# Optimization experiments

Measured on AMD Instinct MI355X. Metric: run time of the kernel, lower is better.

## Reference

```python
import jax, jax.numpy as jnp
import numpy as np

IN_CH = 256
OUT_CH = 256
K = 3
STRIDE = 1
PAD = 1
NUM_EMB = 8


def setup_inputs() -> dict:
    key = jax.random.key(0)
    ks = jax.random.split(key, 6)
    B, H, W = 16, 64, 64
    x = jax.random.normal(ks[0], (B, IN_CH, H, W), dtype=jnp.float32)
    kernal_embed = jax.random.normal(ks[1], (NUM_EMB, IN_CH, OUT_CH, K, K), dtype=jnp.float32)
    # 1x1 conv params (stored as a dense [out,in] matrix) + bias
    cls_conv_w = jax.random.normal(ks[2], (IN_CH, IN_CH), dtype=jnp.float32) / np.sqrt(IN_CH)
    cls_conv_b = jax.random.normal(ks[3], (IN_CH,), dtype=jnp.float32) * 0.01
    cls_dense_w = jax.random.normal(ks[4], (NUM_EMB, IN_CH), dtype=jnp.float32) / np.sqrt(IN_CH)
    cls_dense_b = jax.random.normal(ks[5], (NUM_EMB,), dtype=jnp.float32) * 0.01
    return {"x": x, "kernal_embed": kernal_embed, "cls_conv_w": cls_conv_w,
            "cls_conv_b": cls_conv_b, "cls_dense_w": cls_dense_w, "cls_dense_b": cls_dense_b}


def reference(x, kernal_embed, cls_conv_w, cls_conv_b, cls_dense_w, cls_dense_b):
    B, C, H, W = x.shape
    # 1x1 conv -> global avg pool -> dense -> softmax weights over embeddings
    w = jnp.einsum('bchw,dc->bdhw', x, cls_conv_w) + cls_conv_b[None, :, None, None]
    pooled = jnp.mean(w, axis=(2, 3))                       # (B, C)
    logits = pooled @ cls_dense_w.T + cls_dense_b           # (B, E)
    mix = jax.nn.softmax(logits, axis=1)                    # (B, E)
    # Per-sample kernel synthesis: (B, in, out, k, k)
    kern = jnp.einsum('be,eiojk->biojk', mix, kernal_embed)
    # Faithful to torch .view(-1, in, k, k): raw reshape (mixes in/out axes as in original)
    kern = kern.reshape(B, OUT_CH, IN_CH, K, K)
    # Grouped conv with groups=B == per-sample conv via vmap
    def conv1(xi, wi):
        # xi: (C, H, W), wi: (out, in, k, k)
        return jax.lax.conv_general_dilated(
            xi[None], wi, window_strides=(STRIDE, STRIDE),
            padding=[(PAD, PAD), (PAD, PAD)],
            dimension_numbers=('NCHW', 'OIHW', 'NCHW'))[0]
    out = jax.vmap(conv1)(x, kern)                          # (B, out, H, W)
    return out
```

## Files before the change

kernel.cpp:

```cpp
#include <hip/hip_runtime.h>
#include <stdint.h>

#define B_  16
#define C_  256
#define H_  64
#define W_  64
#define P_  4096
#define E_  8
#define HP_ 66

typedef __bf16 bf16x8 __attribute__((ext_vector_type(8)));
typedef float  f32x4  __attribute__((ext_vector_type(4)));

__device__ __forceinline__ unsigned short f2bf(float f) {
    union { float f; unsigned int u; } v; v.f = f;
    unsigned int u = v.u;
    unsigned int r = (u + 0x7fffu + ((u >> 16) & 1u)) >> 16;
    return (unsigned short)r;
}

__device__ __forceinline__ void async_load16(const void* g, void* l) {
    __builtin_amdgcn_global_load_lds(
        (const __attribute__((address_space(1))) void*)g,
        (__attribute__((address_space(3))) void*)l, 16, 0, 0);
}

__global__ void k_xpose(const float* __restrict__ x, unsigned short* __restrict__ Xp,
                        float* __restrict__ xsum) {
    const int bid = blockIdx.x;
    const int tid = threadIdx.x;

    if (bid < 520) {
        const int gid = bid * 256 + tid;
        const int pix = gid >> 5;
        const int chunk = gid & 31;
        const int bb = pix / 260;
        const int j = pix - bb * 260;
        int h, w;
        if (j < 66)       { h = 0;  w = j; }
        else if (j < 132) { h = 65; w = j - 66; }
        else { int jj = j - 132; h = 1 + (jj & 63); w = (jj < 64) ? 0 : 65; }
        const uint4 z = {0u, 0u, 0u, 0u};
        *(uint4*)(Xp + ((size_t)((bb * HP_ + h) * HP_ + w) << 8) + chunk * 8) = z;
    }

    const int b  = bid >> 8;
    const int h  = (bid >> 2) & 63;
    const int cg = bid & 3;
    const int c0 = cg << 6;
    __shared__ float tile[64][65];
    {
        const int ci = tid >> 2, wseg = tid & 3;
        const float* src = x + ((size_t)(b * 256 + c0 + ci) << 12) + (h << 6) + wseg * 16;
        float s = 0.f;
#pragma unroll
        for (int i = 0; i < 4; ++i) {
            float4 v = *(const float4*)(src + i * 4);
            tile[ci][wseg * 16 + i * 4 + 0] = v.x;
            tile[ci][wseg * 16 + i * 4 + 1] = v.y;
            tile[ci][wseg * 16 + i * 4 + 2] = v.z;
            tile[ci][wseg * 16 + i * 4 + 3] = v.w;
            s += v.x + v.y + v.z + v.w;
        }
        s += __shfl_down(s, 1, 64);
        s += __shfl_down(s, 2, 64);
        if ((tid & 3) == 0) atomicAdd(&xsum[b * 256 + c0 + ci], s);
    }
    __syncthreads();
    {
        const int w = tid >> 2, cs = tid & 3;
        unsigned short ov[16] __attribute__((aligned(16)));
#pragma unroll
        for (int k = 0; k < 16; ++k) ov[k] = f2bf(tile[cs * 16 + k][w]);
        unsigned short* dst = Xp + ((size_t)((b * HP_ + h + 1) * HP_ + (w + 1)) << 8) + c0 + cs * 16;
        ((uint4*)dst)[0] = ((const uint4*)ov)[0];
        ((uint4*)dst)[1] = ((const uint4*)ov)[1];
    }
}

__global__ void k_mix(const float* __restrict__ xsum,
                      const float* __restrict__ cw, const float* __restrict__ cb,
                      const float* __restrict__ dw, const float* __restrict__ db,
                      float* __restrict__ mix) {
    const int b = blockIdx.x, tid = threadIdx.x;
    __shared__ __align__(16) float sxm[256];
    __shared__ __align__(16) float spool[256];
    __shared__ float sl[8];
    sxm[tid] = xsum[b * 256 + tid] * (1.0f / P_);
    __syncthreads();
    {
        float a = cb[tid];
        const float4* cwr = (const float4*)(cw + (size_t)tid * 256);
        const float4* xv4 = (const float4*)sxm;
#pragma unroll 8
        for (int c = 0; c < 64; ++c) {
            const float4 wv = cwr[c];
            const float4 xv = xv4[c];
            a += wv.x * xv.x + wv.y * xv.y + wv.z * xv.z + wv.w * xv.w;
        }
        spool[tid] = a;
    }
    __syncthreads();
    if (tid < 64) {
        const int e = tid >> 3, dl = tid & 7;
        float part = 0.f;
#pragma unroll 4
        for (int d = dl; d < 256; d += 8) part += dw[e * 256 + d] * spool[d];
        part += __shfl_down(part, 4, 64);
        part += __shfl_down(part, 2, 64);
        part += __shfl_down(part, 1, 64);
        if (dl == 0) sl[e] = part + db[e];
    }
    __syncthreads();
    if (tid < 8) {
        float m = sl[0];
        for (int e = 1; e < 8; ++e) m = fmaxf(m, sl[e]);
        float den = 0.f;
        for (int e = 0; e < 8; ++e) den += __expf(sl[e] - m);
        mix[b * 8 + tid] = __expf(sl[tid] - m) / den;
    }
}

__global__ void k_mixkern(const float* __restrict__ KE, const float* __restrict__ mix,
                          unsigned short* __restrict__ Wg) {
    const int o    = blockIdx.x >> 1;
    const int half = blockIdx.x & 1;
    const int ic0  = half << 7;
    const int tid  = threadIdx.x;
    __shared__ __align__(16) float s[8][1152];
    __shared__ float smix[128];
    if (tid < 128) smix[tid] = mix[tid];
#pragma unroll
    for (int e = 0; e < 8; ++e) {
        const float4* src = (const float4*)(KE + (size_t)(e * 256 + o) * 2304 + ic0 * 9);
        float4* dst = (float4*)s[e];
        dst[tid] = src[tid];
        if (tid < 32) dst[256 + tid] = src[256 + tid];
    }
    __syncthreads();
    const int icl = tid & 127;
    const int b0  = (tid >> 7) << 3;
#pragma unroll
    for (int t = 0; t < 9; ++t) {
        float v[8];
#pragma unroll
        for (int e = 0; e < 8; ++e) v[e] = s[e][icl * 9 + t];
#pragma unroll
        for (int bb = 0; bb < 8; ++bb) {
            const int b = b0 + bb;
            float acc = 0.f;
#pragma unroll
            for (int e = 0; e < 8; ++e) acc += smix[b * 8 + e] * v[e];
            Wg[((size_t)(b * 256 + o) * 9 + t) * 256 + ic0 + icl] = f2bf(acc);
        }
    }
}

__global__ __launch_bounds__(512, 2) void k_gemm(const unsigned short* __restrict__ Wg,
                                                 const unsigned short* __restrict__ Xp,
                                                 float* __restrict__ out) {
    __shared__ __align__(16) unsigned short L[4][16384];
    const int tid = threadIdx.x;
    const int bid = blockIdx.x;
    const int xcd = bid & 7;
    const int g   = bid >> 3;
    const int b   = xcd + ((g >> 4) << 3);
    const int tile = g & 15;
    const int h0  = tile << 2;

    const int wid  = tid >> 6;
    const int lane = tid & 63;
    const int wm   = wid >> 2;
    const int wn   = wid & 3;
    const int ql   = lane & 15;
    const int quad = lane >> 4;
    const int sw   = ql & 7;

    const int srow = tid >> 3;
    const int csrc = (tid & 7) ^ (srow & 7);

    f32x4 acc[8][4];
#pragma unroll
    for (int i = 0; i < 8; ++i)
#pragma unroll
        for (int j = 0; j < 4; ++j) acc[i][j] = (f32x4)0.0f;

    auto stageA = [&](int s, int P) {
        const int t = s >> 2, kc = s & 3;
        const unsigned short* ga = Wg + ((size_t)(b * 256 + srow) * 9 + t) * 256
                                   + kc * 64 + csrc * 8;
#pragma unroll
        for (int j = 0; j < 4; ++j)
            async_load16(ga + (size_t)j * 64 * 9 * 256, (char*)L[P] + tid * 16 + j * 8192);
    };
    auto stageB = [&](int s, int P) {
        const int t = s >> 2, kc = s & 3;
        const int kh = t / 3, kw = t - kh * 3;
#pragma unroll
        for (int j = 0; j < 4; ++j)
            async_load16(Xp + (((size_t)((b * HP_ + h0 + j + kh) * HP_ + (srow + kw))) << 8)
                             + kc * 64 + csrc * 8,
                         (char*)L[2 + P] + tid * 16 + j * 8192);
    };

    bf16x8 af[4], bv[4];

#define PH(AP, BP, KK, MH, READB, PREF_STMT, VM_STMT)                              \
    do {                                                                           \
        _Pragma("unroll")                                                          \
        for (int r_ = 0; r_ < 4; ++r_)                                             \
            af[r_] = *(const bf16x8*)((const char*)L[AP]                           \
                     + (wm * 128 + ((MH) * 4 + r_) * 16 + ql) * 128                \
                     + (((((KK) << 2) | quad) ^ sw) << 4));                        \
        if (READB) {                                                               \
            _Pragma("unroll")                                                      \
            for (int r_ = 0; r_ < 4; ++r_)                                         \
                bv[r_] = *(const bf16x8*)((const char*)L[BP]                       \
                         + (wn * 64 + r_ * 16 + ql) * 128                          \
                         + (((((KK) << 2) | quad) ^ sw) << 4));                    \
        }                                                                          \
        PREF_STMT;                                                                 \
        VM_STMT;                                                                   \
        asm volatile("s_barrier" ::: "memory");                                    \
        asm volatile("s_waitcnt lgkmcnt(0)" ::: "memory");                         \
        __builtin_amdgcn_s_setprio(1);                                             \
        _Pragma("unroll")                                                          \
        for (int r_ = 0; r_ < 4; ++r_)                                             \
            _Pragma("unroll")                                                      \
            for (int n_ = 0; n_ < 4; ++n_)                                         \
                acc[(MH) * 4 + r_][n_] = __builtin_amdgcn_mfma_f32_16x16x32_bf16(  \
                    af[r_], bv[n_], acc[(MH) * 4 + r_][n_], 0, 0, 0);              \
        __builtin_amdgcn_s_setprio(0);                                             \
    } while (0)

    stageA(0, 0); stageB(0, 0); stageB(1, 1);
    asm volatile("s_waitcnt vmcnt(4)" ::: "memory");
    asm volatile("s_barrier" ::: "memory");

    for (int i = 0; i < 18; ++i) {
        const int sE = 2 * i;
        const int sO = sE + 1;
        const bool pf = (i < 17);
        PH(0, 2, 0, 0, 1, stageA(sO, 1), ((void)0));
        PH(0, 2, 0, 1, 0, ((void)0), ((void)0));
        PH(0, 2, 1, 0, 1, ((void)0), ((void)0));
        PH(0, 2, 1, 1, 0,
           if (pf) stageB(sE + 2, 0),
           if (pf) { asm volatile("s_waitcnt vmcnt(4)" ::: "memory"); }
           else    { asm volatile("s_waitcnt vmcnt(0)" ::: "memory"); });
        PH(1, 3, 0, 0, 1, if (pf) stageA(sE + 2, 0), ((void)0));
        PH(1, 3, 0, 1, 0, ((void)0), ((void)0));
        PH(1, 3, 1, 0, 1, ((void)0), ((void)0));
        PH(1, 3, 1, 1, 0,
           if (pf) stageB(sO + 2, 1),
           if (pf) { asm volatile("s_waitcnt vmcnt(4)" ::: "memory"); });
    }
#undef PH

#pragma unroll
    for (int m = 0; m < 8; ++m) {
        const int o = wm * 128 + m * 16 + quad * 4;
#pragma unroll
        for (int n = 0; n < 4; ++n) {
            const int w = n * 16 + ql;
            float* po = out + ((size_t)(b * 256 + o) << 12) + ((h0 + wn) << 6) + w;
#pragma unroll
            for (int r = 0; r < 4; ++r) po[(size_t)r << 12] = acc[m][n][r];
        }
    }
}

extern "C" void kernel_launch(void* const* d_in, const int* in_sizes, int n_in,
                              void* d_out, int out_size, void* d_ws, size_t ws_size,
                              hipStream_t stream) {
    const float* x  = (const float*)d_in[0];
    const float* KE = (const float*)d_in[1];
    const float* cw = (const float*)d_in[2];
    const float* cb = (const float*)d_in[3];
    const float* dw = (const float*)d_in[4];
    const float* db = (const float*)d_in[5];
    float* out = (float*)d_out;

    char* ws = (char*)d_ws;
    float* xsum           = (float*)(ws + 0);
    float* mix            = (float*)(ws + 16384);
    unsigned short* Wg    = (unsigned short*)(ws + 32768);
    unsigned short* Xp    = (unsigned short*)(ws + 32768 + 18874368);

    hipMemsetAsync(xsum, 0, B_ * C_ * sizeof(float), stream);
    k_xpose  <<<dim3(B_ * H_ * 4),    dim3(256), 0, stream>>>(x, Xp, xsum);
    k_mix    <<<dim3(B_),             dim3(256), 0, stream>>>(xsum, cw, cb, dw, db, mix);
    k_mixkern<<<dim3(C_ * 2),         dim3(256), 0, stream>>>(KE, mix, Wg);
    k_gemm   <<<dim3(256),            dim3(512), 0, stream>>>(Wg, Xp, out);
}
```

Before: 248.2 us.

## Merge GEMM phases into larger 32-MFMA steps with combined A/B prefetch

Replaces the eight 16-MFMA phases per iteration with four 32-MFMA phases. Each phase now loads both M-halves of A and the B fragment, which halves the number of barriers per K-step. The prefetch schedule changes so that A and B for the next stage are issued together, with full vmcnt(0) drains instead of partial vmcnt(4) waits. This trades more registers and a shallower load pipeline (stalls on all outstanding loads) for fewer synchronisations and better MFMA density.

```diff
diff --git a/kernel.cpp b/kernel.cpp
--- a/kernel.cpp
+++ b/kernel.cpp
@@ -203,22 +203,25 @@
                          (char*)L[2 + P] + tid * 16 + j * 8192);
     };
 
-    bf16x8 af[4], bv[4];
-
-#define PH(AP, BP, KK, MH, READB, PREF_STMT, VM_STMT)                              \
+    bf16x8 af0[4], af1[4], bv[4];
+
+#define MPH(AP, BP, KK, PREF_STMT, VM_STMT)                                        \
     do {                                                                           \
         _Pragma("unroll")                                                          \
         for (int r_ = 0; r_ < 4; ++r_)                                             \
-            af[r_] = *(const bf16x8*)((const char*)L[AP]                           \
-                     + (wm * 128 + ((MH) * 4 + r_) * 16 + ql) * 128                \
+            af0[r_] = *(const bf16x8*)((const char*)L[AP]                          \
+                      + (wm * 128 + r_ * 16 + ql) * 128                            \
+                      + (((((KK) << 2) | quad) ^ sw) << 4));                       \
+        _Pragma("unroll")                                                          \
+        for (int r_ = 0; r_ < 4; ++r_)                                             \
+            af1[r_] = *(const bf16x8*)((const char*)L[AP]                          \
+                      + (wm * 128 + 64 + r_ * 16 + ql) * 128                       \
+                      + (((((KK) << 2) | quad) ^ sw) << 4));                       \
+        _Pragma("unroll")                                                          \
+        for (int r_ = 0; r_ < 4; ++r_)                                             \
+            bv[r_] = *(const bf16x8*)((const char*)L[BP]                           \
+                     + (wn * 64 + r_ * 16 + ql) * 128                              \
                      + (((((KK) << 2) | quad) ^ sw) << 4));                        \
-        if (READB) {                                                               \
-            _Pragma("unroll")                                                      \
-            for (int r_ = 0; r_ < 4; ++r_)                                         \
-                bv[r_] = *(const bf16x8*)((const char*)L[BP]                       \
-                         + (wn * 64 + r_ * 16 + ql) * 128                          \
-                         + (((((KK) << 2) | quad) ^ sw) << 4));                    \
-        }                                                                          \
         PREF_STMT;                                                                 \
         VM_STMT;                                                                   \
         asm volatile("s_barrier" ::: "memory");                                    \
@@ -228,44 +231,44 @@
         for (int r_ = 0; r_ < 4; ++r_)                                             \
             _Pragma("unroll")                                                      \
             for (int n_ = 0; n_ < 4; ++n_)                                         \
-                acc[(MH) * 4 + r_][n_] = __builtin_amdgcn_mfma_f32_16x16x32_bf16(  \
-                    af[r_], bv[n_], acc[(MH) * 4 + r_][n_], 0, 0, 0);              \
+                acc[r_][n_] = __builtin_amdgcn_mfma_f32_16x16x32_bf16(             \
+                    af0[r_], bv[n_], acc[r_][n_], 0, 0, 0);                        \
+        _Pragma("unroll")                                                          \
+        for (int r_ = 0; r_ < 4; ++r_)                                             \
+            _Pragma("unroll")                                                      \
+            for (int n_ = 0; n_ < 4; ++n_)                                         \
+                acc[4 + r_][n_] = __builtin_amdgcn_mfma_f32_16x16x32_bf16(         \
+                    af1[r_], bv[n_], acc[4 + r_][n_], 0, 0, 0);                    \
         __builtin_amdgcn_s_setprio(0);                                             \
     } while (0)
 
-    stageA(0, 0); stageB(0, 0); stageB(1, 1);
-    asm volatile("s_waitcnt vmcnt(4)" ::: "memory");
+    stageA(0, 0); stageB(0, 0);
+    asm volatile("s_waitcnt vmcnt(0)" ::: "memory");
     asm volatile("s_barrier" ::: "memory");
 
     for (int i = 0; i < 18; ++i) {
         const int sE = 2 * i;
         const int sO = sE + 1;
         const bool pf = (i < 17);
-        PH(0, 2, 0, 0, 1, stageA(sO, 1), ((void)0));
-        PH(0, 2, 0, 1, 0, ((void)0), ((void)0));
-        PH(0, 2, 1, 0, 1, ((void)0), ((void)0));
-        PH(0, 2, 1, 1, 0,
-           if (pf) stageB(sE + 2, 0),
-           if (pf) { asm volatile("s_waitcnt vmcnt(4)" ::: "memory"); }
-           else    { asm volatile("s_waitcnt vmcnt(0)" ::: "memory"); });
-        PH(1, 3, 0, 0, 1, if (pf) stageA(sE + 2, 0), ((void)0));
-        PH(1, 3, 0, 1, 0, ((void)0), ((void)0));
-        PH(1, 3, 1, 0, 1, ((void)0), ((void)0));
-        PH(1, 3, 1, 1, 0,
-           if (pf) stageB(sO + 2, 1),
-           if (pf) { asm volatile("s_waitcnt vmcnt(4)" ::: "memory"); });
-    }
-#undef PH
+        MPH(0, 2, 0, { stageA(sO, 1); stageB(sO, 1); }, ((void)0));
+        MPH(0, 2, 1, ((void)0),
+            { asm volatile("s_waitcnt vmcnt(0)" ::: "memory"); });
+        MPH(1, 3, 0, if (pf) { stageA(sE + 2, 0); stageB(sE + 2, 0); }, ((void)0));
+        MPH(1, 3, 1, ((void)0),
+            if (pf) { asm volatile("s_waitcnt vmcnt(0)" ::: "memory"); });
+    }
+#undef MPH
 
 #pragma unroll
     for (int m = 0; m < 8; ++m) {
-        const int o = wm * 128 + m * 16 + quad * 4;
+        const int mh = m >> 2, mr = m & 3;
+        const int o = wm * 128 + mh * 64 + mr * 16 + quad * 4;
 #pragma unroll
         for (int n = 0; n < 4; ++n) {
             const int w = n * 16 + ql;
             float* po = out + ((size_t)(b * 256 + o) << 12) + ((h0 + wn) << 6) + w;
 #pragma unroll
-            for (int r = 0; r < 4; ++r) po[(size_t)r << 12] = acc[m][n][r];
+            for (int r = 0; r < 4; ++r) po[(size_t)r << 12] = acc[mh * 4 + mr][n][r];
         }
     }
 }
```

After: 246.4 us. About the same (-0.7%).
